# Kernel optimization log

Measured on AMD Instinct MI355X. Metric: run time of the kernel, lower is better.

The kernel has to match this reference:

```python
import jax, jax.numpy as jnp
import numpy as np

INPUT_DIM = 1024
ATTN_DIM = 1024
B, S = 4, 4096


def setup_inputs() -> dict:
    key = jax.random.key(0)
    ks = jax.random.split(key, 9)
    def xavier(k, shape):
        fan_in, fan_out = shape[1], shape[0]
        limit = (6.0 / (fan_in + fan_out)) ** 0.5
        return jax.random.uniform(k, shape, jnp.float32, -limit, limit)
    return {
        "x": jax.random.normal(ks[0], (B, S, INPUT_DIM), jnp.float32),
        "Wq": xavier(ks[1], (ATTN_DIM, INPUT_DIM)),
        "bq": jnp.zeros((ATTN_DIM,), jnp.float32),
        "Wk": xavier(ks[2], (ATTN_DIM, INPUT_DIM)),
        "bk": jnp.zeros((ATTN_DIM,), jnp.float32),
        "Wv": xavier(ks[3], (ATTN_DIM, INPUT_DIM)),
        "bv": jnp.zeros((ATTN_DIM,), jnp.float32),
        "Wo": xavier(ks[4], (INPUT_DIM, ATTN_DIM)),
        "bo": jnp.zeros((INPUT_DIM,), jnp.float32),
    }


def reference(x, Wq, bq, Wk, bk, Wv, bv, Wo, bo):
    # Linear layers: y = x @ W^T + b (torch convention, W is [out, in])
    q = jnp.einsum("bsd,ad->bsa", x, Wq) + bq  # [B,S,A]
    k = jnp.einsum("bsd,ad->bsa", x, Wk) + bk
    v = jnp.einsum("bsd,ad->bsa", x, Wv) + bv
    scale = 1.0 / jnp.sqrt(jnp.float32(q.shape[-1]))
    scores = jnp.einsum("bqa,bka->bqk", q, k) * scale  # [B,S,S] full score matrix
    attn = jax.nn.softmax(scores, axis=-1)
    ctx = jnp.einsum("bqk,bka->bqa", attn, v)  # [B,S,A]
    return jnp.einsum("bsa,da->bsd", ctx, Wo) + bo
```

## Files before the change

kernel.cpp:

```cpp
#include <hip/hip_runtime.h>
#include <hip/hip_bf16.h>
#include <cstdint>

#define GLOBAL_AS __attribute__((address_space(1)))
#define LDS_AS    __attribute__((address_space(3)))

typedef __bf16 v8bf __attribute__((ext_vector_type(8)));
typedef __bf16 v4bf __attribute__((ext_vector_type(4)));
typedef float  v4f  __attribute__((ext_vector_type(4)));

struct P2 { __bf16* p[2]; };
struct P4 { __bf16* p[4]; };

#define BAR()   __builtin_amdgcn_s_barrier()
#define LGKM0() asm volatile("s_waitcnt lgkmcnt(0)" ::: "memory")
#define VMC6()  asm volatile("s_waitcnt vmcnt(6)" ::: "memory")

template <int SWZ, int LBN, int LBM, int LNZ>
__device__ __forceinline__ void remap(int& bn, int& bm, int& bz) {
    if constexpr (!SWZ) {
        bn = blockIdx.x; bm = blockIdx.y; bz = blockIdx.z;
    } else {
        const unsigned f = blockIdx.x + (blockIdx.y << LBN) + (blockIdx.z << (LBN + LBM));
        const unsigned xcd = f & 7u, slot = f >> 3;
        constexpr unsigned T = (1u << (LNZ + LBM)) >> 3;
        const unsigned p = xcd * T + (slot >> LBN);
        bn = (int)(slot & ((1u << LBN) - 1u));
        bm = (int)(p & ((1u << LBM) - 1u));
        bz = (int)(p >> LBM);
    }
}

template <int IB, int JB>
__device__ __forceinline__ void mmq(v4f (&acc)[8][4], const v8bf (&As)[4][2],
                                    const v8bf (&Bs)[2][2]) {
    __builtin_amdgcn_s_setprio(1);
#pragma unroll
    for (int i = 0; i < 4; ++i)
#pragma unroll
        for (int j = 0; j < 2; ++j)
#pragma unroll
            for (int ks = 0; ks < 2; ++ks)
                acc[IB + i][JB + j] = __builtin_amdgcn_mfma_f32_16x16x32_bf16(
                    As[i][ks], Bs[j][ks], acc[IB + i][JB + j], 0, 0, 0);
    __builtin_amdgcn_s_setprio(0);
}

__device__ __forceinline__ void kloop256(
    const __bf16* __restrict__ A, int lda,
    const __bf16* __restrict__ B, int ldb, int K,
    __bf16* lds, v4f (&acc)[8][4], int tid)
{
    const int wave = tid >> 6, lane = tid & 63;
    const int quad = lane >> 4, l15 = lane & 15;
    const int wm = wave >> 2, wn = wave & 3;

    const int ce = (((tid & 7) ^ ((tid >> 3) & 7)) << 3);
    int ldsoff[2]; size_t offA[2], offB[2];
#pragma unroll
    for (int l = 0; l < 2; ++l) {
        const int rr = (l * 512 + tid) >> 3;
        offA[l] = (size_t)(((rr & ~63) << 1) + (rr & 63)) * lda + ce;
        offB[l] = (size_t)(((rr & ~31) << 1) + (rr & 31)) * ldb + ce;
        ldsoff[l] = (l * 512 + wave * 64) * 8;
    }
    const __bf16* Ah1 = A + (size_t)64 * lda;
    const __bf16* Bh1 = B + (size_t)32 * ldb;

    auto stA = [&](const __bf16* G, int kt, __bf16* region) {
#pragma unroll
        for (int l = 0; l < 2; ++l)
            __builtin_amdgcn_global_load_lds(
                (const GLOBAL_AS void*)(G + offA[l] + kt),
                (LDS_AS void*)(region + ldsoff[l]), 16, 0, 0);
    };
    auto stB = [&](const __bf16* G, int kt, __bf16* region) {
#pragma unroll
        for (int l = 0; l < 2; ++l)
            __builtin_amdgcn_global_load_lds(
                (const GLOBAL_AS void*)(G + offB[l] + kt),
                (LDS_AS void*)(region + ldsoff[l]), 16, 0, 0);
    };

    const int qsw = (quad << 4) ^ ((l15 & 7) << 4);
    const int laneA0 = ((wm * 64 + l15) << 7) + qsw;
    const int laneA1 = laneA0 ^ 64;
    const int laneB0 = ((wn * 32 + l15) << 7) + qsw;
    const int laneB1 = laneB0 ^ 64;

    v8bf Aset[4][2], Ba[2][2], Bb[2][2];
    auto ldA = [&](const __bf16* region) {
        const char* p = (const char*)region;
#pragma unroll
        for (int i = 0; i < 4; ++i) {
            Aset[i][0] = *(const v8bf*)(p + laneA0 + i * 2048);
            Aset[i][1] = *(const v8bf*)(p + laneA1 + i * 2048);
        }
    };
    auto ldB = [&](const __bf16* region, v8bf (&Bs)[2][2]) {
        const char* p = (const char*)region;
#pragma unroll
        for (int j = 0; j < 2; ++j) {
            Bs[j][0] = *(const v8bf*)(p + laneB0 + j * 2048);
            Bs[j][1] = *(const v8bf*)(p + laneB1 + j * 2048);
        }
    };

    __bf16* const Ra0 = lds;
    __bf16* const Ra1 = lds + 8192;
    __bf16* const Rb0 = lds + 16384;
    __bf16* const Rb1 = lds + 24576;
    __bf16* const Sa0 = lds + 32768;
    __bf16* const Sa1 = lds + 40960;
    __bf16* const Sb0 = lds + 49152;
    __bf16* const Sb1 = lds + 57344;

    const int NT = K >> 6;
    const int kcap = K - 64;

    stA(A, 0, Ra0); stB(B, 0, Rb0); stB(Bh1, 0, Rb1); stA(Ah1, 0, Ra1);
    stA(A, 64, Sa0); stB(B, 64, Sb0); stB(Bh1, 64, Sb1);
    VMC6(); BAR();

    for (int it = 0; it < (NT >> 1); ++it) {
        const int u = it << 1;
        int ktA = (u + 2) << 6; if (ktA > kcap) ktA = kcap;
        int ktB = (u + 3) << 6; if (ktB > kcap) ktB = kcap;
        const int kt1 = (u + 1) << 6;
        ldA(Ra0); ldB(Rb0, Ba);
        stA(Ah1, kt1, Sa1);
        LGKM0();
        mmq<0, 0>(acc, Aset, Ba);
        BAR();
        ldB(Rb1, Bb);
        stA(A, ktA, Ra0);
        LGKM0();
        mmq<0, 2>(acc, Aset, Bb);
        BAR();
        ldA(Ra1);
        stB(B, ktA, Rb0);
        LGKM0();
        mmq<4, 2>(acc, Aset, Bb);
        BAR();
        stB(Bh1, ktA, Rb1);
        LGKM0();
        mmq<4, 0>(acc, Aset, Ba);
        VMC6(); BAR();
        ldA(Sa0); ldB(Sb0, Ba);
        stA(Ah1, ktA, Ra1);
        LGKM0();
        mmq<0, 0>(acc, Aset, Ba);
        BAR();
        ldB(Sb1, Bb);
        stA(A, ktB, Sa0);
        LGKM0();
        mmq<0, 2>(acc, Aset, Bb);
        BAR();
        ldA(Sa1);
        stB(B, ktB, Sb0);
        LGKM0();
        mmq<4, 2>(acc, Aset, Bb);
        BAR();
        stB(Bh1, ktB, Sb1);
        LGKM0();
        mmq<4, 0>(acc, Aset, Ba);
        VMC6(); BAR();
    }
}

template <typename OutT, int SWZ, int LBN, int LBM, int LNZ>
__global__ __launch_bounds__(512, 2)
void gemm_bt(const __bf16* __restrict__ A, int lda, long long sA,
             const __bf16* __restrict__ B, int ldb, long long sB,
             OutT* __restrict__ C, int ldc, long long sC,
             int K,
             const float* __restrict__ bias_col,
             const float* __restrict__ bias_row)
{
    __shared__ __align__(16) __bf16 lds[2 * 4 * 8192];
    const int tid = threadIdx.x, wave = tid >> 6, lane = tid & 63;
    const int quad = lane >> 4, l15 = lane & 15;
    const int wm = wave >> 2, wn = wave & 3;
    int bn, bm, bz;
    remap<SWZ, LBN, LBM, LNZ>(bn, bm, bz);
    A += (long long)bz * sA;
    B += (long long)bz * sB;
    C += (long long)bz * sC;

    v4f acc[8][4];
#pragma unroll
    for (int i = 0; i < 8; ++i)
#pragma unroll
        for (int j = 0; j < 4; ++j) acc[i][j] = (v4f){0.f, 0.f, 0.f, 0.f};

    kloop256(A + (size_t)bm * 256 * lda, lda, B + (size_t)bn * 256 * ldb, ldb,
             K, lds, acc, tid);

#pragma unroll
    for (int i = 0; i < 8; ++i) {
        const int row0 = bm * 256 + wm * 128 + i * 16 + quad * 4;
#pragma unroll
        for (int j = 0; j < 4; ++j) {
            const int col = bn * 256 + wn * 64 + j * 16 + l15;
            const float bc = bias_col ? bias_col[col] : 0.f;
#pragma unroll
            for (int r = 0; r < 4; ++r) {
                float v = acc[i][j][r] + bc;
                if (bias_row) v += bias_row[row0 + r];
                C[(size_t)(row0 + r) * ldc + col] = (OutT)v;
            }
        }
    }
}

template <int SWZ, int LBN, int LBM, int LNZ>
__global__ __launch_bounds__(512, 2)
void gemm_exp(const __bf16* __restrict__ A, int lda, long long sA,
              const __bf16* __restrict__ B, int ldb, long long sB,
              P2 Eout, int ldc,
              float* __restrict__ rowsum, int rsStride, int K)
{
    __shared__ __align__(16) __bf16 lds[2 * 4 * 8192];
    const int tid = threadIdx.x, wave = tid >> 6, lane = tid & 63;
    const int quad = lane >> 4, l15 = lane & 15;
    const int wm = wave >> 2, wn = wave & 3;
    int bn, bm, bz;
    remap<SWZ, LBN, LBM, LNZ>(bn, bm, bz);
    A += (long long)bz * sA;
    B += (long long)bz * sB;
    __bf16* C = Eout.p[bz];
    float* rs = rowsum + (long long)bz * rsStride;

    v4f acc[8][4];
#pragma unroll
    for (int i = 0; i < 8; ++i)
#pragma unroll
        for (int j = 0; j < 4; ++j) acc[i][j] = (v4f){0.f, 0.f, 0.f, 0.f};

    kloop256(A + (size_t)bm * 256 * lda, lda, B + (size_t)bn * 256 * ldb, ldb,
             K, lds, acc, tid);

#pragma unroll
    for (int i = 0; i < 8; ++i) {
        const int row0 = bm * 256 + wm * 128 + i * 16 + quad * 4;
        float part[4] = {0.f, 0.f, 0.f, 0.f};
#pragma unroll
        for (int j = 0; j < 4; ++j) {
            const int col = bn * 256 + wn * 64 + j * 16 + l15;
#pragma unroll
            for (int r = 0; r < 4; ++r) {
                float e = __expf(acc[i][j][r]);
                C[(size_t)(row0 + r) * ldc + col] = (__bf16)e;
                part[r] += e;
            }
        }
#pragma unroll
        for (int r = 0; r < 4; ++r) {
#pragma unroll
            for (int off = 1; off < 16; off <<= 1)
                part[r] += __shfl_xor(part[r], off, 16);
        }
        if (l15 == 0) {
#pragma unroll
            for (int r = 0; r < 4; ++r) atomicAdd(&rs[row0 + r], part[r]);
        }
    }
}

template <int SWZ, int LBN, int LBM, int LNZ>
__global__ __launch_bounds__(512, 2)
void gemm_av(P4 Ain, int lda,
             const __bf16* __restrict__ Bv, int ldb, long long sB,
             __bf16* __restrict__ C, int ldc, long long sC,
             const float* __restrict__ rowsum, int rsStride, int K)
{
    __shared__ __align__(16) __bf16 lds[2 * 4 * 8192];
    const int tid = threadIdx.x, wave = tid >> 6, lane = tid & 63;
    const int quad = lane >> 4, l15 = lane & 15;
    const int wm = wave >> 2, wn = wave & 3;
    int bn, bm, bz;
    remap<SWZ, LBN, LBM, LNZ>(bn, bm, bz);
    const __bf16* A = Ain.p[bz];
    const __bf16* B = Bv + (long long)bz * sB;
    C += (long long)bz * sC;
    const float* rs = rowsum + (long long)bz * rsStride;

    v4f acc[8][4];
#pragma unroll
    for (int i = 0; i < 8; ++i)
#pragma unroll
        for (int j = 0; j < 4; ++j) acc[i][j] = (v4f){0.f, 0.f, 0.f, 0.f};

    kloop256(A + (size_t)bm * 256 * lda, lda, B + (size_t)bn * 256 * ldb, ldb,
             K, lds, acc, tid);

#pragma unroll
    for (int i = 0; i < 8; ++i) {
        const int row0 = bm * 256 + wm * 128 + i * 16 + quad * 4;
        float inv[4];
#pragma unroll
        for (int r = 0; r < 4; ++r) inv[r] = 1.0f / rs[row0 + r];
#pragma unroll
        for (int j = 0; j < 4; ++j) {
            const int col = bn * 256 + wn * 64 + j * 16 + l15;
#pragma unroll
            for (int r = 0; r < 4; ++r)
                C[(size_t)(row0 + r) * ldc + col] = (__bf16)(acc[i][j][r] * inv[r]);
        }
    }
}

__global__ void cvt_f32_bf16(const float* __restrict__ in, __bf16* __restrict__ out, int n4) {
    int i = blockIdx.x * blockDim.x + threadIdx.x;
    if (i >= n4) return;
    float4 f = ((const float4*)in)[i];
    v4bf o;
    o[0] = (__bf16)f.x; o[1] = (__bf16)f.y; o[2] = (__bf16)f.z; o[3] = (__bf16)f.w;
    ((v4bf*)out)[i] = o;
}

__global__ void cvt_w4(const float* __restrict__ w0, const float* __restrict__ w1,
                       const float* __restrict__ w2, const float* __restrict__ w3,
                       __bf16* __restrict__ dst, int n4, float wscale0) {
    const float* s = blockIdx.y == 0 ? w0 : blockIdx.y == 1 ? w1 : blockIdx.y == 2 ? w2 : w3;
    const float sc = blockIdx.y == 0 ? wscale0 : 1.f;
    int i = blockIdx.x * blockDim.x + threadIdx.x;
    if (i >= n4) return;
    float4 f = ((const float4*)s)[i];
    v4bf o;
    o[0] = (__bf16)(f.x * sc); o[1] = (__bf16)(f.y * sc);
    o[2] = (__bf16)(f.z * sc); o[3] = (__bf16)(f.w * sc);
    ((v4bf*)(dst + (size_t)blockIdx.y * n4 * 4))[i] = o;
}

__global__ void concat_bias2(const float* __restrict__ b0, const float* __restrict__ b1,
                             float* __restrict__ dst, int n, float s0) {
    int i = blockIdx.x * blockDim.x + threadIdx.x;
    if (i < n) dst[i] = b0[i] * s0;
    else if (i < 2 * n) dst[i] = b1[i - n];
}

__global__ void zero_f32(float* __restrict__ p, int n) {
    int i = blockIdx.x * blockDim.x + threadIdx.x;
    if (i < n) p[i] = 0.f;
}

extern "C" void kernel_launch(void* const* d_in, const int* in_sizes, int n_in,
                              void* d_out, int out_size, void* d_ws, size_t ws_size,
                              hipStream_t stream)
{
    const float* x  = (const float*)d_in[0];
    const float* Wq = (const float*)d_in[1];
    const float* bq = (const float*)d_in[2];
    const float* Wk = (const float*)d_in[3];
    const float* bk = (const float*)d_in[4];
    const float* Wv = (const float*)d_in[5];
    const float* bv = (const float*)d_in[6];
    const float* Wo = (const float*)d_in[7];
    const float* bo = (const float*)d_in[8];
    float* out = (float*)d_out;

    constexpr int B = 4, S = 4096, D = 1024;
    constexpr long long MS = (long long)B * S;
    constexpr float scale = 0.03125f;

    char* w = (char*)d_ws;
    size_t used = 0;
    auto alloc = [&](size_t bytes) -> char* {
        char* p = w + used;
        used += (bytes + 255) & ~(size_t)255;
        return p;
    };
    __bf16* xb  = (__bf16*)alloc((size_t)MS * D * 2);
    __bf16* wqb = (__bf16*)alloc(4 * (size_t)D * D * 2);
    __bf16* wvb = wqb + 2 * (size_t)D * D;
    __bf16* wob = wqb + 3 * (size_t)D * D;
    float*  bqk = (float*)alloc(2 * D * 4);
    float*  rsm = (float*)alloc((size_t)B * S * 4);
    __bf16* qk  = (__bf16*)alloc((size_t)MS * 2 * D * 2);
    __bf16* vT  = (__bf16*)alloc((size_t)D * MS * 2);
    __bf16* Efr = (__bf16*)alloc(3 * (size_t)S * S * 2);
    __bf16* ctx = xb;
    if (used > ws_size) return;

    const long long SS = (long long)S * S;
    const long long qs = (long long)S * 2 * D;

    zero_f32<<<(B * S + 255) / 256, 256, 0, stream>>>(rsm, B * S);
    {
        int n4 = (int)(MS * D / 4);
        cvt_f32_bf16<<<(n4 + 255) / 256, 256, 0, stream>>>(x, xb, n4);
    }
    cvt_w4<<<dim3(D * D / 4 / 256, 4), 256, 0, stream>>>(Wq, Wk, Wv, Wo, wqb, D * D / 4, scale);
    concat_bias2<<<(2 * D + 255) / 256, 256, 0, stream>>>(bq, bk, bqk, D, scale);

    const dim3 blk(512);
    gemm_bt<__bf16, 1, 3, 6, 0><<<dim3(2 * D / 256, MS / 256), blk, 0, stream>>>(
        xb, D, 0, wqb, D, 0, qk, 2 * D, 0, D, bqk, nullptr);
    gemm_bt<__bf16, 0, 0, 0, 0><<<dim3(MS / 256, D / 256), blk, 0, stream>>>(
        wvb, D, 0, xb, D, 0, vT, (int)MS, 0, D, nullptr, bv);

    P2 e0; e0.p[0] = Efr;          e0.p[1] = Efr + SS;
    P2 e1; e1.p[0] = Efr + 2 * SS; e1.p[1] = qk;
    gemm_exp<1, 4, 4, 1><<<dim3(S / 256, S / 256, 2), blk, 0, stream>>>(
        qk, 2 * D, qs, qk + D, 2 * D, qs, e0, S, rsm, S, D);
    gemm_exp<1, 4, 4, 1><<<dim3(S / 256, S / 256, 2), blk, 0, stream>>>(
        qk + 2 * qs, 2 * D, qs, qk + D + 2 * qs, 2 * D, qs, e1, S, rsm + 2 * S, S, D);

    P4 ea; ea.p[0] = Efr; ea.p[1] = Efr + SS; ea.p[2] = Efr + 2 * SS; ea.p[3] = qk;
    gemm_av<1, 2, 4, 2><<<dim3(D / 256, S / 256, B), blk, 0, stream>>>(
        ea, S, vT, (int)MS, S, ctx, D, (long long)S * D, rsm, S, S);

    gemm_bt<float, 1, 2, 6, 0><<<dim3(D / 256, MS / 256), blk, 0, stream>>>(
        ctx, D, 0, wob, D, 0, out, D, 0, D, bo, nullptr);
}
```

Baseline: 584.0 us.

## Double-buffer LDS-to-register fragments and drop explicit lgkmcnt waits in GEMM loop

```diff
diff --git a/kernel.cpp b/kernel.cpp
--- a/kernel.cpp
+++ b/kernel.cpp
@@ -13,7 +13,6 @@
 struct P4 { __bf16* p[4]; };
 
 #define BAR()   __builtin_amdgcn_s_barrier()
-#define LGKM0() asm volatile("s_waitcnt lgkmcnt(0)" ::: "memory")
 #define VMC6()  asm volatile("s_waitcnt vmcnt(6)" ::: "memory")
 
 template <int SWZ, int LBN, int LBM, int LNZ>
@@ -88,21 +87,21 @@
     const int laneB0 = ((wn * 32 + l15) << 7) + qsw;
     const int laneB1 = laneB0 ^ 64;
 
-    v8bf Aset[4][2], Ba[2][2], Bb[2][2];
-    auto ldA = [&](const __bf16* region) {
+    v8bf A0[4][2], A1[4][2], B0[2][2], B1[2][2];
+    auto ldA = [&](const __bf16* region, v8bf (&Ad)[4][2]) {
         const char* p = (const char*)region;
 #pragma unroll
         for (int i = 0; i < 4; ++i) {
-            Aset[i][0] = *(const v8bf*)(p + laneA0 + i * 2048);
-            Aset[i][1] = *(const v8bf*)(p + laneA1 + i * 2048);
+            Ad[i][0] = *(const v8bf*)(p + laneA0 + i * 2048);
+            Ad[i][1] = *(const v8bf*)(p + laneA1 + i * 2048);
         }
     };
-    auto ldB = [&](const __bf16* region, v8bf (&Bs)[2][2]) {
+    auto ldB = [&](const __bf16* region, v8bf (&Bd)[2][2]) {
         const char* p = (const char*)region;
 #pragma unroll
         for (int j = 0; j < 2; ++j) {
-            Bs[j][0] = *(const v8bf*)(p + laneB0 + j * 2048);
-            Bs[j][1] = *(const v8bf*)(p + laneB1 + j * 2048);
+            Bd[j][0] = *(const v8bf*)(p + laneB0 + j * 2048);
+            Bd[j][1] = *(const v8bf*)(p + laneB1 + j * 2048);
         }
     };
 
@@ -121,50 +120,47 @@
     stA(A, 0, Ra0); stB(B, 0, Rb0); stB(Bh1, 0, Rb1); stA(Ah1, 0, Ra1);
     stA(A, 64, Sa0); stB(B, 64, Sb0); stB(Bh1, 64, Sb1);
     VMC6(); BAR();
+    ldA(Ra0, A0); ldB(Rb0, B0);
 
     for (int it = 0; it < (NT >> 1); ++it) {
         const int u = it << 1;
         int ktA = (u + 2) << 6; if (ktA > kcap) ktA = kcap;
         int ktB = (u + 3) << 6; if (ktB > kcap) ktB = kcap;
         const int kt1 = (u + 1) << 6;
-        ldA(Ra0); ldB(Rb0, Ba);
         stA(Ah1, kt1, Sa1);
-        LGKM0();
-        mmq<0, 0>(acc, Aset, Ba);
-        BAR();
-        ldB(Rb1, Bb);
+        ldB(Rb1, B1);
+        mmq<0, 0>(acc, A0, B0);
+        BAR();
         stA(A, ktA, Ra0);
-        LGKM0();
-        mmq<0, 2>(acc, Aset, Bb);
-        BAR();
-        ldA(Ra1);
+        ldA(Ra1, A1);
+        mmq<0, 2>(acc, A0, B1);
+        BAR();
         stB(B, ktA, Rb0);
-        LGKM0();
-        mmq<4, 2>(acc, Aset, Bb);
+        mmq<4, 2>(acc, A1, B1);
         BAR();
         stB(Bh1, ktA, Rb1);
-        LGKM0();
-        mmq<4, 0>(acc, Aset, Ba);
-        VMC6(); BAR();
-        ldA(Sa0); ldB(Sb0, Ba);
+        VMC6();
+        ldA(Sa0, A0);
+        mmq<4, 0>(acc, A1, B0);
+        ldB(Sb0, B0);
+        BAR();
         stA(Ah1, ktA, Ra1);
-        LGKM0();
-        mmq<0, 0>(acc, Aset, Ba);
-        BAR();
-        ldB(Sb1, Bb);
+        ldB(Sb1, B1);
+        mmq<0, 0>(acc, A0, B0);
+        BAR();
         stA(A, ktB, Sa0);
-        LGKM0();
-        mmq<0, 2>(acc, Aset, Bb);
-        BAR();
-        ldA(Sa1);
+        ldA(Sa1, A1);
+        mmq<0, 2>(acc, A0, B1);
+        BAR();
         stB(B, ktB, Sb0);
-        LGKM0();
-        mmq<4, 2>(acc, Aset, Bb);
+        mmq<4, 2>(acc, A1, B1);
         BAR();
         stB(Bh1, ktB, Sb1);
-        LGKM0();
-        mmq<4, 0>(acc, Aset, Ba);
-        VMC6(); BAR();
+        VMC6();
+        ldA(Ra0, A0);
+        mmq<4, 0>(acc, A1, B0);
+        ldB(Rb0, B0);
+        BAR();
     }
 }
 
```

Result: faster. 558.3 us (-4.4%).
